# Optimization experiments

Measured on AMD Instinct MI355X. Metric: run time of the kernel, lower is better.

The kernel has to match this reference:

```python
import jax, jax.numpy as jnp
import numpy as np

N_NODES = 50000
N_EDGES = 800000
F_IN = 128
HEADS = 8
C_OUT = 16  # per-head out channels; HEADS*C_OUT = 128
NEG_SLOPE = 0.2
LN_EPS = 1e-5


def setup_inputs() -> dict:
    key = jax.random.key(0)
    ks = jax.random.split(key, 10)
    HC = HEADS * C_OUT
    x = jax.random.normal(ks[0], (N_NODES, F_IN), dtype=jnp.float32)
    edge_index = jax.random.randint(ks[1], (2, N_EDGES), 0, N_NODES, dtype=jnp.int32)
    # GATConv params (PyG defaults: lin has no bias, att vectors per head, output bias)
    W = jax.random.normal(ks[2], (F_IN, HC), dtype=jnp.float32) / np.sqrt(F_IN)
    att_src = jax.random.normal(ks[3], (HEADS, C_OUT), dtype=jnp.float32) / np.sqrt(C_OUT)
    att_dst = jax.random.normal(ks[4], (HEADS, C_OUT), dtype=jnp.float32) / np.sqrt(C_OUT)
    conv_bias = jnp.zeros((HC,), dtype=jnp.float32)
    ln_g = jnp.ones((HC,), dtype=jnp.float32)
    ln_b = jnp.zeros((HC,), dtype=jnp.float32)
    ff_w = jax.random.normal(ks[5], (HC, F_IN), dtype=jnp.float32) / np.sqrt(HC)
    ff_b = jnp.zeros((F_IN,), dtype=jnp.float32)
    return dict(x=x, edge_index=edge_index, W=W, att_src=att_src, att_dst=att_dst,
                conv_bias=conv_bias, ln_g=ln_g, ln_b=ln_b, ff_w=ff_w, ff_b=ff_b)


def reference(x, edge_index, W, att_src, att_dst, conv_bias, ln_g, ln_b, ff_w, ff_b):
    N = x.shape[0]
    H, C = att_src.shape
    # add self loops (PyG GATConv default)
    loop = jnp.arange(N, dtype=edge_index.dtype)
    src = jnp.concatenate([edge_index[0], loop])  # [E+N]
    dst = jnp.concatenate([edge_index[1], loop])
    # linear transform, per-head view
    h = (x @ W).reshape(N, H, C)  # [N,H,C]
    # per-node attention logits, then gather per edge
    a_s = jnp.einsum('nhc,hc->nh', h, att_src)  # [N,H]
    a_d = jnp.einsum('nhc,hc->nh', h, att_dst)
    e = jax.nn.leaky_relu(a_s[src] + a_d[dst], NEG_SLOPE)  # [E+N, H]
    # segment softmax over destination neighborhoods (every node has a self loop)
    emax = jax.ops.segment_max(e, dst, num_segments=N)  # [N,H]
    ex = jnp.exp(e - emax[dst])
    denom = jax.ops.segment_sum(ex, dst, num_segments=N)  # [N,H]
    alpha = ex / denom[dst]  # [E+N, H]
    # weighted scatter-aggregate of source messages
    msg = alpha[:, :, None] * h[src]  # [E+N, H, C]
    out = jax.ops.segment_sum(msg, dst, num_segments=N).reshape(N, H * C) + conv_bias
    # LayerNorm
    mu = out.mean(-1, keepdims=True)
    var = out.var(-1, keepdims=True)
    out = (out - mu) * jax.lax.rsqrt(var + LN_EPS) * ln_g + ln_b
    # feed-forward + residual
    out = out @ ff_w + ff_b
    return x + out
```

## Files before the change

kernel.cpp:

```cpp
#include <hip/hip_runtime.h>
#include <hip/hip_fp16.h>

#define F 128
#define NEG_SLOPE 0.2f
#define LN_EPS 1e-5f
#define LDA 136

typedef _Float16 f16;
typedef _Float16 f16x8 __attribute__((ext_vector_type(8)));
typedef float f32x4 __attribute__((ext_vector_type(4)));

__global__ __launch_bounds__(256) void conv_w(const float* __restrict__ W,
                                              const float* __restrict__ ffw,
                                              __half* __restrict__ Wt,
                                              __half* __restrict__ ffwt) {
    int idx = blockIdx.x * 256 + threadIdx.x;
    int which = idx >> 14;
    int t = idx & 16383;
    int k = t >> 7, c = t & 127;
    const float* s = which ? ffw : W;
    __half* d = which ? ffwt : Wt;
    d[c * 128 + k] = __float2half(s[t]);
}

__global__ __launch_bounds__(256) void init_deg(int* __restrict__ deg, int N) {
    int i = blockIdx.x * 256 + threadIdx.x;
    if (i < N) deg[i] = 0;
}

__global__ __launch_bounds__(256) void count_deg(const int* __restrict__ dst,
                                                 int* __restrict__ deg, int E) {
    int i = blockIdx.x * 256 + threadIdx.x;
    if (i < E) atomicAdd(&deg[dst[i]], 1);
}

__global__ __launch_bounds__(256) void scan_k1(const int* __restrict__ deg,
                                               int* __restrict__ bsum, int N) {
    __shared__ int tmp[256];
    int t = threadIdx.x;
    int i = blockIdx.x * 256 + t;
    tmp[t] = (i < N) ? (deg[i] + 1) : 0;
    __syncthreads();
    for (int off = 128; off > 0; off >>= 1) {
        if (t < off) tmp[t] += tmp[t + off];
        __syncthreads();
    }
    if (t == 0) bsum[blockIdx.x] = tmp[0];
}

__global__ __launch_bounds__(256) void scan_k2(const int* __restrict__ bsum,
                                               int* __restrict__ bpre,
                                               int* __restrict__ offsets,
                                               int nb, int N) {
    __shared__ int tmp[256];
    int t = threadIdx.x;
    int v = (t < nb) ? bsum[t] : 0;
    tmp[t] = v;
    __syncthreads();
    for (int off = 1; off < 256; off <<= 1) {
        int u = (t >= off) ? tmp[t - off] : 0;
        __syncthreads();
        tmp[t] += u;
        __syncthreads();
    }
    if (t < nb) bpre[t] = tmp[t] - v;
    if (t == 255) offsets[N] = tmp[255];
}

__global__ __launch_bounds__(256) void scan_k3(const int* __restrict__ deg,
                                               const int* __restrict__ bpre,
                                               int* __restrict__ offsets, int N) {
    __shared__ int tmp[256];
    int t = threadIdx.x;
    int i = blockIdx.x * 256 + t;
    int v = (i < N) ? (deg[i] + 1) : 0;
    tmp[t] = v;
    __syncthreads();
    for (int off = 1; off < 256; off <<= 1) {
        int u = (t >= off) ? tmp[t - off] : 0;
        __syncthreads();
        tmp[t] += u;
        __syncthreads();
    }
    if (i < N) offsets[i] = bpre[blockIdx.x] + tmp[t] - v;
}

__global__ __launch_bounds__(256) void fill_self(const int* __restrict__ offsets,
                                                 int* __restrict__ cursor,
                                                 int* __restrict__ csr, int N) {
    int i = blockIdx.x * 256 + threadIdx.x;
    if (i < N) {
        int o = offsets[i];
        csr[o] = i;
        cursor[i] = o + 1;
    }
}

__global__ __launch_bounds__(256) void fill_edges(const int* __restrict__ src,
                                                  const int* __restrict__ dst,
                                                  int* __restrict__ cursor,
                                                  int* __restrict__ csr, int E) {
    int i = blockIdx.x * 256 + threadIdx.x;
    if (i < E) {
        int p = atomicAdd(&cursor[dst[i]], 1);
        csr[p] = src[i];
    }
}

template <int MODE>
__global__ __launch_bounds__(256) void gemm_mfma(const float* __restrict__ Af,
                                                 const __half* __restrict__ Ah,
                                                 const __half* __restrict__ Bt,
                                                 const float* __restrict__ bias,
                                                 const float* __restrict__ resid,
                                                 __half* __restrict__ outH,
                                                 float* __restrict__ outF,
                                                 int M) {
    __shared__ f16 As[64 * LDA];
    __shared__ f16 Bs[128 * LDA];
    int tid = threadIdx.x;
    int row0 = blockIdx.x * 64;

    for (int c = tid; c < 128 * 16; c += 256) {
        int r = c >> 4, k8 = (c & 15) * 8;
        uint4 v = *(const uint4*)(Bt + r * 128 + k8);
        *(uint4*)(&Bs[r * LDA + k8]) = v;
    }
    if (MODE == 0) {
        for (int c = tid; c < 64 * 32; c += 256) {
            int r = c >> 5, c4 = (c & 31) * 4;
            int gr = row0 + r;
            float4 v = make_float4(0.f, 0.f, 0.f, 0.f);
            if (gr < M) v = *(const float4*)(Af + (size_t)gr * F + c4);
            f16 h0 = (f16)v.x, h1 = (f16)v.y, h2 = (f16)v.z, h3 = (f16)v.w;
            As[r * LDA + c4 + 0] = h0; As[r * LDA + c4 + 1] = h1;
            As[r * LDA + c4 + 2] = h2; As[r * LDA + c4 + 3] = h3;
        }
    } else {
        for (int c = tid; c < 64 * 16; c += 256) {
            int r = c >> 4, k8 = (c & 15) * 8;
            int gr = row0 + r;
            uint4 v = make_uint4(0, 0, 0, 0);
            if (gr < M) v = *(const uint4*)(Ah + (size_t)gr * F + k8);
            *(uint4*)(&As[r * LDA + k8]) = v;
        }
    }
    __syncthreads();

    int wave = tid >> 6, l = tid & 63;
    int r0 = wave * 16;
    int lr = l & 15, lk = (l >> 4) * 8;

    f32x4 acc[8];
#pragma unroll
    for (int f = 0; f < 8; f++) acc[f] = (f32x4){0.f, 0.f, 0.f, 0.f};

#pragma unroll
    for (int ks = 0; ks < 128; ks += 32) {
        f16x8 a = *(const f16x8*)(&As[(r0 + lr) * LDA + ks + lk]);
#pragma unroll
        for (int f = 0; f < 8; f++) {
            f16x8 b = *(const f16x8*)(&Bs[(f * 16 + lr) * LDA + ks + lk]);
            acc[f] = __builtin_amdgcn_mfma_f32_16x16x32_f16(a, b, acc[f], 0, 0, 0);
        }
    }

#pragma unroll
    for (int f = 0; f < 8; f++) {
        int col = f * 16 + lr;
#pragma unroll
        for (int i = 0; i < 4; i++) {
            int row = row0 + r0 + (l >> 4) * 4 + i;
            if (row < M) {
                if (MODE == 0) {
                    outH[(size_t)row * F + col] = __float2half(acc[f][i]);
                } else {
                    outF[(size_t)row * F + col] =
                        acc[f][i] + bias[col] + resid[(size_t)row * F + col];
                }
            }
        }
    }
}

__global__ __launch_bounds__(256) void attn_logits(const __half* __restrict__ h16,
                                                   const float* __restrict__ att_src,
                                                   const float* __restrict__ att_dst,
                                                   float* __restrict__ a_s,
                                                   float* __restrict__ a_d, int N) {
    int node = (blockIdx.x * 256 + threadIdx.x) >> 6;
    int l = threadIdx.x & 63;
    if (node >= N) return;
    __half2 hv = *reinterpret_cast<const __half2*>(h16 + (size_t)node * F + l * 2);
    float2 f = __half22float2(hv);
    float s = f.x * att_src[2 * l] + f.y * att_src[2 * l + 1];
    float d = f.x * att_dst[2 * l] + f.y * att_dst[2 * l + 1];
#pragma unroll
    for (int m = 1; m < 8; m <<= 1) {
        s += __shfl_xor(s, m);
        d += __shfl_xor(d, m);
    }
    if ((l & 7) == 0) {
        a_s[node * 8 + (l >> 3)] = s;
        a_d[node * 8 + (l >> 3)] = d;
    }
}

__global__ __launch_bounds__(256) void aggregate(const __half* __restrict__ h16,
                                                 const float* __restrict__ a_s,
                                                 const float* __restrict__ a_d,
                                                 const int* __restrict__ offsets,
                                                 const int* __restrict__ csr,
                                                 const float* __restrict__ conv_bias,
                                                 float* __restrict__ gat, int N) {
    int node = (blockIdx.x * 256 + threadIdx.x) >> 6;
    if (node >= N) return;
    int lane = threadIdx.x & 63;
    int half = lane >> 5, l5 = lane & 31;
    int c0 = l5 * 4, head = l5 >> 2;

    float ad = a_d[node * 8 + head];
    float m = -1e30f, s = 0.f;
    float a0 = 0.f, a1 = 0.f, a2 = 0.f, a3 = 0.f;
    int beg = offsets[node], end = offsets[node + 1];
    int steps = (end - beg + 1) >> 1;

    for (int t = 0; t < steps; t++) {
        int idx = beg + 2 * t + half;
        bool act = idx < end;
        int src = csr[act ? idx : beg];
        float e = a_s[src * 8 + head] + ad;
        e = (e > 0.f) ? e : NEG_SLOPE * e;
        float ee = act ? e : -1e30f;
        float mn = fmaxf(m, ee);
        float c = __expf(m - mn);
        float p = act ? __expf(ee - mn) : 0.f;
        uint2 hv = *(const uint2*)(h16 + (size_t)src * F + c0);
        __half2 u0 = *reinterpret_cast<__half2*>(&hv.x);
        __half2 u1 = *reinterpret_cast<__half2*>(&hv.y);
        float2 f0 = __half22float2(u0);
        float2 f1 = __half22float2(u1);
        s = s * c + p;
        a0 = a0 * c + p * f0.x;
        a1 = a1 * c + p * f0.y;
        a2 = a2 * c + p * f1.x;
        a3 = a3 * c + p * f1.y;
        m = mn;
    }
    float mo = __shfl_xor(m, 32);
    float mn = fmaxf(m, mo);
    float ca = __expf(m - mn), cb = __expf(mo - mn);
    float so = __shfl_xor(s, 32);
    float b0 = __shfl_xor(a0, 32), b1 = __shfl_xor(a1, 32);
    float b2 = __shfl_xor(a2, 32), b3 = __shfl_xor(a3, 32);
    s = s * ca + so * cb;
    a0 = a0 * ca + b0 * cb;
    a1 = a1 * ca + b1 * cb;
    a2 = a2 * ca + b2 * cb;
    a3 = a3 * ca + b3 * cb;
    if (half == 0) {
        float inv = 1.f / s;
        float4 o;
        o.x = a0 * inv + conv_bias[c0 + 0];
        o.y = a1 * inv + conv_bias[c0 + 1];
        o.z = a2 * inv + conv_bias[c0 + 2];
        o.w = a3 * inv + conv_bias[c0 + 3];
        *(float4*)(gat + (size_t)node * F + c0) = o;
    }
}

__global__ __launch_bounds__(256) void layernorm(const float* __restrict__ gat,
                                                 const float* __restrict__ g,
                                                 const float* __restrict__ b,
                                                 __half* __restrict__ ln16, int N) {
    int node = (blockIdx.x * 256 + threadIdx.x) >> 6;
    int l = threadIdx.x & 63;
    if (node >= N) return;
    float2 v = *(const float2*)(gat + (size_t)node * F + l * 2);
    float s = v.x + v.y, sq = v.x * v.x + v.y * v.y;
#pragma unroll
    for (int m = 1; m < 64; m <<= 1) {
        s += __shfl_xor(s, m);
        sq += __shfl_xor(sq, m);
    }
    float mu = s * (1.f / F);
    float var = sq * (1.f / F) - mu * mu;
    float rs = rsqrtf(var + LN_EPS);
    float o0 = (v.x - mu) * rs * g[2 * l] + b[2 * l];
    float o1 = (v.y - mu) * rs * g[2 * l + 1] + b[2 * l + 1];
    *reinterpret_cast<__half2*>(ln16 + (size_t)node * F + l * 2) = __floats2half2_rn(o0, o1);
}

extern "C" void kernel_launch(void* const* d_in, const int* in_sizes, int n_in,
                              void* d_out, int out_size, void* d_ws, size_t ws_size,
                              hipStream_t stream) {
    const float* x         = (const float*)d_in[0];
    const int*   ei        = (const int*)d_in[1];
    const float* W         = (const float*)d_in[2];
    const float* att_src   = (const float*)d_in[3];
    const float* att_dst   = (const float*)d_in[4];
    const float* conv_bias = (const float*)d_in[5];
    const float* ln_g      = (const float*)d_in[6];
    const float* ln_b      = (const float*)d_in[7];
    const float* ff_w      = (const float*)d_in[8];
    const float* ff_b      = (const float*)d_in[9];
    float* out = (float*)d_out;

    int N = in_sizes[0] / F;
    int E = in_sizes[1] / 2;
    const int* srcp = ei;
    const int* dstp = ei + E;

    char* ws = (char*)d_ws;
    __half* h16 = (__half*)ws;  ws += (size_t)N * F * 2;
    float* gat  = (float*)ws;   ws += (size_t)N * F * 4;
    float* a_s  = (float*)ws;   ws += (size_t)N * 8 * 4;
    float* a_d  = (float*)ws;   ws += (size_t)N * 8 * 4;
    int* deg    = (int*)ws;     ws += (size_t)N * 4;
    int* offs   = (int*)ws;     ws += (size_t)(N + 1) * 4 + 12;
    int* cursor = (int*)ws;     ws += (size_t)N * 4;
    int* csr    = (int*)ws;     ws += (size_t)(E + N) * 4;
    int* bsum   = (int*)ws;     ws += 256 * 4;
    int* bpre   = (int*)ws;     ws += 256 * 4;
    __half* Wt16  = (__half*)ws; ws += 16384 * 2;
    __half* ffwt16= (__half*)ws; ws += 16384 * 2;
    __half* ln16 = h16;

    int nwb  = (N + 3) / 4;
    int ngb  = (N + 63) / 64;
    int n256 = (N + 255) / 256;
    int e256 = (E + 255) / 256;
    int nb   = n256;

    hipLaunchKernelGGL(init_deg, dim3(n256), dim3(256), 0, stream, deg, N);
    hipLaunchKernelGGL(conv_w, dim3(128), dim3(256), 0, stream, W, ff_w, Wt16, ffwt16);
    hipLaunchKernelGGL((gemm_mfma<0>), dim3(ngb), dim3(256), 0, stream,
                       x, (const __half*)nullptr, Wt16, nullptr, nullptr, h16, nullptr, N);
    hipLaunchKernelGGL(attn_logits, dim3(nwb), dim3(256), 0, stream,
                       h16, att_src, att_dst, a_s, a_d, N);
    hipLaunchKernelGGL(count_deg, dim3(e256), dim3(256), 0, stream, dstp, deg, E);
    hipLaunchKernelGGL(scan_k1, dim3(nb), dim3(256), 0, stream, deg, bsum, N);
    hipLaunchKernelGGL(scan_k2, dim3(1), dim3(256), 0, stream, bsum, bpre, offs, nb, N);
    hipLaunchKernelGGL(scan_k3, dim3(nb), dim3(256), 0, stream, deg, bpre, offs, N);
    hipLaunchKernelGGL(fill_self, dim3(n256), dim3(256), 0, stream, offs, cursor, csr, N);
    hipLaunchKernelGGL(fill_edges, dim3(e256), dim3(256), 0, stream, srcp, dstp, cursor, csr, E);
    hipLaunchKernelGGL(aggregate, dim3(nwb), dim3(256), 0, stream,
                       h16, a_s, a_d, offs, csr, conv_bias, gat, N);
    hipLaunchKernelGGL(layernorm, dim3(nwb), dim3(256), 0, stream, gat, ln_g, ln_b, ln16, N);
    hipLaunchKernelGGL((gemm_mfma<1>), dim3(ngb), dim3(256), 0, stream,
                       nullptr, ln16, ffwt16, ff_b, x, nullptr, out, N);
}
```

Before: 310.3 us.

## Fuse attention logits into GEMM, aggregation with LayerNorm, and merge prep kernels

Merges deg init with weight conversion, and the scan's final pass with self-loop CSR fill. Attention logits are now computed in the first MFMA GEMM epilogue via lane shuffles, and aggregation is fused with LayerNorm, so the fp32 intermediate is no longer written to or read back from memory. Aggregation now uses 4 edge groups of 16 lanes, each loading 8 halves, and merges their online-softmax states with xor shuffles. This cuts launches and memory traffic, at the cost of more shuffles and registers in the GEMM epilogue and an extra ln16 buffer.

```diff
diff --git a/kernel.cpp b/kernel.cpp
--- a/kernel.cpp
+++ b/kernel.cpp
@@ -10,22 +10,22 @@
 typedef _Float16 f16x8 __attribute__((ext_vector_type(8)));
 typedef float f32x4 __attribute__((ext_vector_type(4)));
 
-__global__ __launch_bounds__(256) void conv_w(const float* __restrict__ W,
-                                              const float* __restrict__ ffw,
-                                              __half* __restrict__ Wt,
-                                              __half* __restrict__ ffwt) {
+__global__ __launch_bounds__(256) void prep(int* __restrict__ deg,
+                                            const float* __restrict__ W,
+                                            const float* __restrict__ ffw,
+                                            __half* __restrict__ Wt,
+                                            __half* __restrict__ ffwt, int N) {
     int idx = blockIdx.x * 256 + threadIdx.x;
-    int which = idx >> 14;
-    int t = idx & 16383;
-    int k = t >> 7, c = t & 127;
-    const float* s = which ? ffw : W;
-    __half* d = which ? ffwt : Wt;
-    d[c * 128 + k] = __float2half(s[t]);
-}
-
-__global__ __launch_bounds__(256) void init_deg(int* __restrict__ deg, int N) {
-    int i = blockIdx.x * 256 + threadIdx.x;
-    if (i < N) deg[i] = 0;
+    if (idx < N) deg[idx] = 0;
+    int t2 = idx - N;
+    if (t2 >= 0 && t2 < 2 * 16384) {
+        int which = t2 >> 14;
+        int t = t2 & 16383;
+        int k = t >> 7, c = t & 127;
+        const float* s = which ? ffw : W;
+        __half* d = which ? ffwt : Wt;
+        d[c * 128 + k] = __float2half(s[t]);
+    }
 }
 
 __global__ __launch_bounds__(256) void count_deg(const int* __restrict__ dst,
@@ -67,9 +67,11 @@
     if (t == 255) offsets[N] = tmp[255];
 }
 
-__global__ __launch_bounds__(256) void scan_k3(const int* __restrict__ deg,
-                                               const int* __restrict__ bpre,
-                                               int* __restrict__ offsets, int N) {
+__global__ __launch_bounds__(256) void scan_k3_fill(const int* __restrict__ deg,
+                                                    const int* __restrict__ bpre,
+                                                    int* __restrict__ offsets,
+                                                    int* __restrict__ cursor,
+                                                    int* __restrict__ csr, int N) {
     __shared__ int tmp[256];
     int t = threadIdx.x;
     int i = blockIdx.x * 256 + t;
@@ -82,15 +84,9 @@
         tmp[t] += u;
         __syncthreads();
     }
-    if (i < N) offsets[i] = bpre[blockIdx.x] + tmp[t] - v;
-}
-
-__global__ __launch_bounds__(256) void fill_self(const int* __restrict__ offsets,
-                                                 int* __restrict__ cursor,
-                                                 int* __restrict__ csr, int N) {
-    int i = blockIdx.x * 256 + threadIdx.x;
     if (i < N) {
-        int o = offsets[i];
+        int o = bpre[blockIdx.x] + tmp[t] - v;
+        offsets[i] = o;
         csr[o] = i;
         cursor[i] = o + 1;
     }
@@ -113,6 +109,10 @@
                                                  const __half* __restrict__ Bt,
                                                  const float* __restrict__ bias,
                                                  const float* __restrict__ resid,
+                                                 const float* __restrict__ att_src,
+                                                 const float* __restrict__ att_dst,
+                                                 float* __restrict__ a_s,
+                                                 float* __restrict__ a_d,
                                                  __half* __restrict__ outH,
                                                  float* __restrict__ outF,
                                                  int M) {
@@ -132,9 +132,8 @@
             int gr = row0 + r;
             float4 v = make_float4(0.f, 0.f, 0.f, 0.f);
             if (gr < M) v = *(const float4*)(Af + (size_t)gr * F + c4);
-            f16 h0 = (f16)v.x, h1 = (f16)v.y, h2 = (f16)v.z, h3 = (f16)v.w;
-            As[r * LDA + c4 + 0] = h0; As[r * LDA + c4 + 1] = h1;
-            As[r * LDA + c4 + 2] = h2; As[r * LDA + c4 + 3] = h3;
+            As[r * LDA + c4 + 0] = (f16)v.x; As[r * LDA + c4 + 1] = (f16)v.y;
+            As[r * LDA + c4 + 2] = (f16)v.z; As[r * LDA + c4 + 3] = (f16)v.w;
         }
     } else {
         for (int c = tid; c < 64 * 16; c += 256) {
@@ -181,52 +180,61 @@
             }
         }
     }
-}
-
-__global__ __launch_bounds__(256) void attn_logits(const __half* __restrict__ h16,
-                                                   const float* __restrict__ att_src,
-                                                   const float* __restrict__ att_dst,
-                                                   float* __restrict__ a_s,
-                                                   float* __restrict__ a_d, int N) {
-    int node = (blockIdx.x * 256 + threadIdx.x) >> 6;
-    int l = threadIdx.x & 63;
-    if (node >= N) return;
-    __half2 hv = *reinterpret_cast<const __half2*>(h16 + (size_t)node * F + l * 2);
-    float2 f = __half22float2(hv);
-    float s = f.x * att_src[2 * l] + f.y * att_src[2 * l + 1];
-    float d = f.x * att_dst[2 * l] + f.y * att_dst[2 * l + 1];
-#pragma unroll
-    for (int m = 1; m < 8; m <<= 1) {
-        s += __shfl_xor(s, m);
-        d += __shfl_xor(d, m);
-    }
-    if ((l & 7) == 0) {
-        a_s[node * 8 + (l >> 3)] = s;
-        a_d[node * 8 + (l >> 3)] = d;
-    }
-}
-
-__global__ __launch_bounds__(256) void aggregate(const __half* __restrict__ h16,
-                                                 const float* __restrict__ a_s,
-                                                 const float* __restrict__ a_d,
-                                                 const int* __restrict__ offsets,
-                                                 const int* __restrict__ csr,
-                                                 const float* __restrict__ conv_bias,
-                                                 float* __restrict__ gat, int N) {
+
+    if (MODE == 0) {
+#pragma unroll
+        for (int f = 0; f < 8; f++) {
+            float av = att_src[f * 16 + lr];
+            float dv = att_dst[f * 16 + lr];
+            float ps0 = acc[f][0] * av, ps1 = acc[f][1] * av,
+                  ps2 = acc[f][2] * av, ps3 = acc[f][3] * av;
+            float pd0 = acc[f][0] * dv, pd1 = acc[f][1] * dv,
+                  pd2 = acc[f][2] * dv, pd3 = acc[f][3] * dv;
+#pragma unroll
+            for (int mask = 1; mask < 16; mask <<= 1) {
+                ps0 += __shfl_xor(ps0, mask); ps1 += __shfl_xor(ps1, mask);
+                ps2 += __shfl_xor(ps2, mask); ps3 += __shfl_xor(ps3, mask);
+                pd0 += __shfl_xor(pd0, mask); pd1 += __shfl_xor(pd1, mask);
+                pd2 += __shfl_xor(pd2, mask); pd3 += __shfl_xor(pd3, mask);
+            }
+            if (lr == 0) {
+                int rbase = row0 + r0 + (l >> 4) * 4;
+                if (rbase + 0 < M) { a_s[(rbase + 0) * 8 + f] = ps0; a_d[(rbase + 0) * 8 + f] = pd0; }
+                if (rbase + 1 < M) { a_s[(rbase + 1) * 8 + f] = ps1; a_d[(rbase + 1) * 8 + f] = pd1; }
+                if (rbase + 2 < M) { a_s[(rbase + 2) * 8 + f] = ps2; a_d[(rbase + 2) * 8 + f] = pd2; }
+                if (rbase + 3 < M) { a_s[(rbase + 3) * 8 + f] = ps3; a_d[(rbase + 3) * 8 + f] = pd3; }
+            }
+        }
+    }
+}
+
+__global__ __launch_bounds__(256) void aggregate_ln(const __half* __restrict__ h16,
+                                                    const float* __restrict__ a_s,
+                                                    const float* __restrict__ a_d,
+                                                    const int* __restrict__ offsets,
+                                                    const int* __restrict__ csr,
+                                                    const float* __restrict__ conv_bias,
+                                                    const float* __restrict__ lng,
+                                                    const float* __restrict__ lnb,
+                                                    __half* __restrict__ ln16, int N) {
     int node = (blockIdx.x * 256 + threadIdx.x) >> 6;
     if (node >= N) return;
-    int lane = threadIdx.x & 63;
-    int half = lane >> 5, l5 = lane & 31;
-    int c0 = l5 * 4, head = l5 >> 2;
+    int l = threadIdx.x & 63;
+    int g = l >> 4, lg = l & 15;
+    int c0 = lg * 8, head = lg >> 1;
 
     float ad = a_d[node * 8 + head];
     float m = -1e30f, s = 0.f;
-    float a0 = 0.f, a1 = 0.f, a2 = 0.f, a3 = 0.f;
+    float acc[8];
+#pragma unroll
+    for (int j = 0; j < 8; j++) acc[j] = 0.f;
+
     int beg = offsets[node], end = offsets[node + 1];
-    int steps = (end - beg + 1) >> 1;
-
+    int steps = (end - beg + 3) >> 2;
+
+#pragma unroll 2
     for (int t = 0; t < steps; t++) {
-        int idx = beg + 2 * t + half;
+        int idx = beg + 4 * t + g;
         bool act = idx < end;
         int src = csr[act ? idx : beg];
         float e = a_s[src * 8 + head] + ad;
@@ -235,60 +243,68 @@
         float mn = fmaxf(m, ee);
         float c = __expf(m - mn);
         float p = act ? __expf(ee - mn) : 0.f;
-        uint2 hv = *(const uint2*)(h16 + (size_t)src * F + c0);
-        __half2 u0 = *reinterpret_cast<__half2*>(&hv.x);
-        __half2 u1 = *reinterpret_cast<__half2*>(&hv.y);
-        float2 f0 = __half22float2(u0);
-        float2 f1 = __half22float2(u1);
+        uint4 hv = *(const uint4*)(h16 + (size_t)src * F + c0);
+        const __half2* hp = reinterpret_cast<const __half2*>(&hv);
+        float2 f0 = __half22float2(hp[0]);
+        float2 f1 = __half22float2(hp[1]);
+        float2 f2 = __half22float2(hp[2]);
+        float2 f3 = __half22float2(hp[3]);
         s = s * c + p;
-        a0 = a0 * c + p * f0.x;
-        a1 = a1 * c + p * f0.y;
-        a2 = a2 * c + p * f1.x;
-        a3 = a3 * c + p * f1.y;
+        acc[0] = acc[0] * c + p * f0.x; acc[1] = acc[1] * c + p * f0.y;
+        acc[2] = acc[2] * c + p * f1.x; acc[3] = acc[3] * c + p * f1.y;
+        acc[4] = acc[4] * c + p * f2.x; acc[5] = acc[5] * c + p * f2.y;
+        acc[6] = acc[6] * c + p * f3.x; acc[7] = acc[7] * c + p * f3.y;
         m = mn;
     }
-    float mo = __shfl_xor(m, 32);
-    float mn = fmaxf(m, mo);
-    float ca = __expf(m - mn), cb = __expf(mo - mn);
-    float so = __shfl_xor(s, 32);
-    float b0 = __shfl_xor(a0, 32), b1 = __shfl_xor(a1, 32);
-    float b2 = __shfl_xor(a2, 32), b3 = __shfl_xor(a3, 32);
-    s = s * ca + so * cb;
-    a0 = a0 * ca + b0 * cb;
-    a1 = a1 * ca + b1 * cb;
-    a2 = a2 * ca + b2 * cb;
-    a3 = a3 * ca + b3 * cb;
-    if (half == 0) {
-        float inv = 1.f / s;
-        float4 o;
-        o.x = a0 * inv + conv_bias[c0 + 0];
-        o.y = a1 * inv + conv_bias[c0 + 1];
-        o.z = a2 * inv + conv_bias[c0 + 2];
-        o.w = a3 * inv + conv_bias[c0 + 3];
-        *(float4*)(gat + (size_t)node * F + c0) = o;
-    }
-}
-
-__global__ __launch_bounds__(256) void layernorm(const float* __restrict__ gat,
-                                                 const float* __restrict__ g,
-                                                 const float* __restrict__ b,
-                                                 __half* __restrict__ ln16, int N) {
-    int node = (blockIdx.x * 256 + threadIdx.x) >> 6;
-    int l = threadIdx.x & 63;
-    if (node >= N) return;
-    float2 v = *(const float2*)(gat + (size_t)node * F + l * 2);
-    float s = v.x + v.y, sq = v.x * v.x + v.y * v.y;
-#pragma unroll
-    for (int m = 1; m < 64; m <<= 1) {
-        s += __shfl_xor(s, m);
-        sq += __shfl_xor(sq, m);
-    }
-    float mu = s * (1.f / F);
+
+#pragma unroll
+    for (int mask = 16; mask <= 32; mask <<= 1) {
+        float mo = __shfl_xor(m, mask);
+        float mn = fmaxf(m, mo);
+        float ca = __expf(m - mn), cb = __expf(mo - mn);
+        float so = __shfl_xor(s, mask);
+        s = s * ca + so * cb;
+#pragma unroll
+        for (int j = 0; j < 8; j++) {
+            float ao = __shfl_xor(acc[j], mask);
+            acc[j] = acc[j] * ca + ao * cb;
+        }
+        m = mn;
+    }
+
+    float inv = 1.f / s;
+    float4 cb0 = *(const float4*)(conv_bias + c0);
+    float4 cb1 = *(const float4*)(conv_bias + c0 + 4);
+    float o[8];
+    o[0] = acc[0] * inv + cb0.x; o[1] = acc[1] * inv + cb0.y;
+    o[2] = acc[2] * inv + cb0.z; o[3] = acc[3] * inv + cb0.w;
+    o[4] = acc[4] * inv + cb1.x; o[5] = acc[5] * inv + cb1.y;
+    o[6] = acc[6] * inv + cb1.z; o[7] = acc[7] * inv + cb1.w;
+
+    float sum = 0.f, sq = 0.f;
+#pragma unroll
+    for (int j = 0; j < 8; j++) { sum += o[j]; sq += o[j] * o[j]; }
+#pragma unroll
+    for (int mask = 1; mask < 16; mask <<= 1) {
+        sum += __shfl_xor(sum, mask);
+        sq  += __shfl_xor(sq, mask);
+    }
+    float mu = sum * (1.f / F);
     float var = sq * (1.f / F) - mu * mu;
     float rs = rsqrtf(var + LN_EPS);
-    float o0 = (v.x - mu) * rs * g[2 * l] + b[2 * l];
-    float o1 = (v.y - mu) * rs * g[2 * l + 1] + b[2 * l + 1];
-    *reinterpret_cast<__half2*>(ln16 + (size_t)node * F + l * 2) = __floats2half2_rn(o0, o1);
+
+    if (g == 0) {
+        float4 g0 = *(const float4*)(lng + c0);
+        float4 g1 = *(const float4*)(lng + c0 + 4);
+        float4 b0 = *(const float4*)(lnb + c0);
+        float4 b1 = *(const float4*)(lnb + c0 + 4);
+        __half2 ph[4];
+        ph[0] = __floats2half2_rn((o[0] - mu) * rs * g0.x + b0.x, (o[1] - mu) * rs * g0.y + b0.y);
+        ph[1] = __floats2half2_rn((o[2] - mu) * rs * g0.z + b0.z, (o[3] - mu) * rs * g0.w + b0.w);
+        ph[2] = __floats2half2_rn((o[4] - mu) * rs * g1.x + b1.x, (o[5] - mu) * rs * g1.y + b1.y);
+        ph[3] = __floats2half2_rn((o[6] - mu) * rs * g1.z + b1.z, (o[7] - mu) * rs * g1.w + b1.w);
+        *(uint4*)(ln16 + (size_t)node * F + c0) = *(uint4*)ph;
+    }
 }
 
 extern "C" void kernel_launch(void* const* d_in, const int* in_sizes, int n_in,
@@ -312,41 +328,38 @@
     const int* dstp = ei + E;
 
     char* ws = (char*)d_ws;
-    __half* h16 = (__half*)ws;  ws += (size_t)N * F * 2;
-    float* gat  = (float*)ws;   ws += (size_t)N * F * 4;
-    float* a_s  = (float*)ws;   ws += (size_t)N * 8 * 4;
-    float* a_d  = (float*)ws;   ws += (size_t)N * 8 * 4;
-    int* deg    = (int*)ws;     ws += (size_t)N * 4;
-    int* offs   = (int*)ws;     ws += (size_t)(N + 1) * 4 + 12;
-    int* cursor = (int*)ws;     ws += (size_t)N * 4;
-    int* csr    = (int*)ws;     ws += (size_t)(E + N) * 4;
-    int* bsum   = (int*)ws;     ws += 256 * 4;
-    int* bpre   = (int*)ws;     ws += 256 * 4;
-    __half* Wt16  = (__half*)ws; ws += 16384 * 2;
-    __half* ffwt16= (__half*)ws; ws += 16384 * 2;
-    __half* ln16 = h16;
+    __half* h16  = (__half*)ws;  ws += (size_t)N * F * 2;
+    __half* ln16 = (__half*)ws;  ws += (size_t)N * F * 2;
+    float* a_s   = (float*)ws;   ws += (size_t)N * 8 * 4;
+    float* a_d   = (float*)ws;   ws += (size_t)N * 8 * 4;
+    int* deg     = (int*)ws;     ws += (size_t)N * 4;
+    int* offs    = (int*)ws;     ws += (size_t)(N + 1) * 4 + 12;
+    int* cursor  = (int*)ws;     ws += (size_t)N * 4;
+    int* csr     = (int*)ws;     ws += (size_t)(E + N) * 4;
+    int* bsum    = (int*)ws;     ws += 256 * 4;
+    int* bpre    = (int*)ws;     ws += 256 * 4;
+    __half* Wt16   = (__half*)ws; ws += 16384 * 2;
+    __half* ffwt16 = (__half*)ws; ws += 16384 * 2;
 
     int nwb  = (N + 3) / 4;
     int ngb  = (N + 63) / 64;
     int n256 = (N + 255) / 256;
     int e256 = (E + 255) / 256;
     int nb   = n256;
-
-    hipLaunchKernelGGL(init_deg, dim3(n256), dim3(256), 0, stream, deg, N);
-    hipLaunchKernelGGL(conv_w, dim3(128), dim3(256), 0, stream, W, ff_w, Wt16, ffwt16);
+    int prep_b = (N + 2 * 16384 + 255) / 256;
+
+    hipLaunchKernelGGL(prep, dim3(prep_b), dim3(256), 0, stream, deg, W, ff_w, Wt16, ffwt16, N);
+    hipLaunchKernelGGL(count_deg, dim3(e256), dim3(256), 0, stream, dstp, deg, E);
     hipLaunchKernelGGL((gemm_mfma<0>), dim3(ngb), dim3(256), 0, stream,
-                       x, (const __half*)nullptr, Wt16, nullptr, nullptr, h16, nullptr, N);
-    hipLaunchKernelGGL(attn_logits, dim3(nwb), dim3(256), 0, stream,
-                       h16, att_src, att_dst, a_s, a_d, N);
-    hipLaunchKernelGGL(count_deg, dim3(e256), dim3(256), 0, stream, dstp, deg, E);
+                       x, (const __half*)nullptr, Wt16, nullptr, nullptr,
+                       att_src, att_dst, a_s, a_d, h16, nullptr, N);
     hipLaunchKernelGGL(scan_k1, dim3(nb), dim3(256), 0, stream, deg, bsum, N);
     hipLaunchKernelGGL(scan_k2, dim3(1), dim3(256), 0, stream, bsum, bpre, offs, nb, N);
-    hipLaunchKernelGGL(scan_k3, dim3(nb), dim3(256), 0, stream, deg, bpre, offs, N);
-    hipLaunchKernelGGL(fill_self, dim3(n256), dim3(256), 0, stream, offs, cursor, csr, N);
+    hipLaunchKernelGGL(scan_k3_fill, dim3(nb), dim3(256), 0, stream, deg, bpre, offs, cursor, csr, N);
     hipLaunchKernelGGL(fill_edges, dim3(e256), dim3(256), 0, stream, srcp, dstp, cursor, csr, E);
-    hipLaunchKernelGGL(aggregate, dim3(nwb), dim3(256), 0, stream,
-                       h16, a_s, a_d, offs, csr, conv_bias, gat, N);
-    hipLaunchKernelGGL(layernorm, dim3(nwb), dim3(256), 0, stream, gat, ln_g, ln_b, ln16, N);
+    hipLaunchKernelGGL(aggregate_ln, dim3(nwb), dim3(256), 0, stream,
+                       h16, a_s, a_d, offs, csr, conv_bias, ln_g, ln_b, ln16, N);
     hipLaunchKernelGGL((gemm_mfma<1>), dim3(ngb), dim3(256), 0, stream,
-                       nullptr, ln16, ffwt16, ff_b, x, nullptr, out, N);
-}
+                       nullptr, ln16, ffwt16, ff_b, x, nullptr, nullptr, nullptr, nullptr,
+                       nullptr, out, N);
+}
```

Measured after the change: 274.7 us. 1.13x faster.
